# Kernel tuning notes

Measured on AMD Instinct MI355X. Metric: run time of the kernel, lower is better.

The kernel has to match this reference:

```python
import jax, jax.numpy as jnp
import numpy as np

LAYERS = (256, 256, 256)
SPLIT = True


def setup_inputs() -> dict:
    key = jax.random.key(0)
    ks = jax.random.split(key, 4)
    B, F0, D = 512, 40, 32
    # field_num with split=True: [40, 128, 128, 128]
    fnum = [F0]
    for i, s in enumerate(LAYERS):
        fnum.append(s // 2 if (SPLIT and i < len(LAYERS) - 1) else (s // 2 if SPLIT else s))
    # conv input channels per layer: fnum[i] * F0
    c1, c2, c3 = fnum[0] * F0, fnum[1] * F0, fnum[2] * F0  # 1600, 5120, 5120
    inputs = jax.random.normal(ks[0], (B, F0, D), dtype=jnp.float32)
    W1 = jax.random.normal(ks[1], (c1, LAYERS[0]), dtype=jnp.float32) / jnp.sqrt(jnp.float32(c1))
    W2 = jax.random.normal(ks[2], (c2, LAYERS[1]), dtype=jnp.float32) / jnp.sqrt(jnp.float32(c2))
    W3 = jax.random.normal(ks[3], (c3, LAYERS[2]), dtype=jnp.float32) / jnp.sqrt(jnp.float32(c3))
    b1 = jnp.zeros((LAYERS[0],), dtype=jnp.float32)
    b2 = jnp.zeros((LAYERS[1],), dtype=jnp.float32)
    b3 = jnp.zeros((LAYERS[2],), dtype=jnp.float32)
    return {"inputs": inputs, "W1": W1, "b1": b1, "W2": W2, "b2": b2, "W3": W3, "b3": b3}


def _cin_forward(inputs, params):
    # inputs: [B, F0, D]
    B, F0, D = inputs.shape
    x0 = inputs
    h = inputs
    outputs = []
    n = len(params)
    for i, (W, b) in enumerate(params):
        # Per-embedding-dim outer product: [B, D, Fi, F0] -> flatten channels.
        z = jnp.einsum('bfd,bgd->bdfg', h, x0).reshape(B, D, -1)
        # 1x1 Conv1D over length-D axis == dense projection on channel axis.
        y = z @ W + b                     # [B, D, size]
        y = jax.nn.relu(y)
        y = jnp.transpose(y, (0, 2, 1))   # [B, size, D]
        if SPLIT and i < n - 1:
            half = y.shape[1] // 2
            outputs.append(y[:, :half, :])
            h = y[:, half:, :]
        else:
            outputs.append(y)
            h = y
    pooled = jnp.concatenate(outputs, axis=1)  # [B, sum_out_fields, D]
    return jnp.sum(pooled, axis=2)             # [B, sum_out_fields]


def reference(inputs, W1, b1, W2, b2, W3, b3):
    return _cin_forward(inputs, [(W1, b1), (W2, b2), (W3, b3)])
```

## Files before the change

### kernel.cpp

```cpp
#include <hip/hip_runtime.h>
#include <hip/hip_bf16.h>


typedef __attribute__((ext_vector_type(8))) short short8;
typedef __attribute__((ext_vector_type(4))) float f32x4;

#define DEVINL __device__ __forceinline__

DEVINL float bf16f(unsigned short u) {
  return __builtin_bit_cast(float, ((unsigned int)u) << 16);
}
DEVINL unsigned short f2bf(float f) {
  unsigned int u = __builtin_bit_cast(unsigned int, f);
  u = u + 0x7FFFu + ((u >> 16) & 1u);
  return (unsigned short)(u >> 16);
}
DEVINL unsigned int pk2(float lo, float hi) {
  union { __hip_bfloat162 h; unsigned int u; } cv;
  cv.h = __float22bfloat162_rn(make_float2(lo, hi));
  return cv.u;
}
DEVINL void gl_lds16(const unsigned short* g, unsigned short* l) {
  __builtin_amdgcn_global_load_lds(
      (const __attribute__((address_space(1))) unsigned int*)g,
      (__attribute__((address_space(3))) unsigned int*)l, 16, 0, 0);
}

__global__ void prep_x(const float* __restrict__ in, unsigned short* __restrict__ xT) {
  __shared__ float lf[40 * 33];
  const int b = blockIdx.x, t = threadIdx.x;
  for (int i = t; i < 1280; i += 256) {
    int g = i >> 5, d = i & 31;
    lf[g * 33 + d] = in[b * 1280 + i];
  }
  __syncthreads();
  for (int i = t; i < 1280; i += 256) {
    int d = i / 40, g = i % 40;
    xT[b * 1280 + i] = f2bf(lf[g * 33 + d]);
  }
}

__global__ void prep_w(const float* __restrict__ W1, const float* __restrict__ W2,
                       const float* __restrict__ W3, unsigned short* __restrict__ Wf1,
                       unsigned short* __restrict__ Wf2, unsigned short* __restrict__ Wf3) {
  __shared__ float lw[8192];
  const int bid = blockIdx.x, t = threadIdx.x;
  const float* W; unsigned short* dst; int s, SPW;
  if (bid < 50)       { W = W1; dst = Wf1; s = bid;       SPW = 10; }
  else if (bid < 210) { W = W2; dst = Wf2; s = bid - 50;  SPW = 32; }
  else                { W = W3; dst = Wf3; s = bid - 210; SPW = 32; }
  const int smod = s % SPW, w = s / SPW;
  for (int i = t; i < 8192; i += 256) {
    int kl = i >> 8, col = i & 255;
    int f = 4 * smod + (kl >> 3);
    int g = 8 * w + (kl & 7);
    lw[i] = W[(f * 40 + g) * 256 + col];
  }
  __syncthreads();
  for (int c = t; c < 1024; c += 256) {
    int grp = c >> 6, ll = c & 63;
    int qq = ll >> 4, col = grp * 16 + (ll & 15);
    unsigned short u[8];
#pragma unroll
    for (int j = 0; j < 8; ++j) u[j] = f2bf(lw[(qq * 8 + j) * 256 + col]);
    uint4 v;
    v.x = (unsigned)u[0] | ((unsigned)u[1] << 16);
    v.y = (unsigned)u[2] | ((unsigned)u[3] << 16);
    v.z = (unsigned)u[4] | ((unsigned)u[5] << 16);
    v.w = (unsigned)u[6] | ((unsigned)u[7] << 16);
    *(uint4*)&dst[s * 8192 + c * 8] = v;
  }
}

template <int LAYER>
__global__ __launch_bounds__(256, 2) void cin_layer(
    const unsigned short* __restrict__ Wfrag, const unsigned short* __restrict__ xT,
    const unsigned short* __restrict__ hIn, const float* __restrict__ bias,
    unsigned short* __restrict__ hOut, float* __restrict__ out) {
  constexpr int FIN = (LAYER == 1) ? 40 : 128;
  constexpr int NKT = FIN * 40 / 32;
  constexpr int SPW = FIN / 4;
  constexpr int HP = 144;

  constexpr int SM_SHORTS = 16384 + 5120 + ((LAYER > 1) ? 128 * HP : 8);
  __shared__ __align__(16) unsigned short smem[SM_SHORTS];
  unsigned short* Bb = smem;
  unsigned short* xs = smem + 16384;
  unsigned short* hs = smem + 16384 + 5120;

  const int tid = threadIdx.x;
  const int l = tid & 63;
  const int wid = tid >> 6;
  const int q = l >> 4;
  const int bm = blockIdx.x >> 2;
  const int tn = blockIdx.x & 3;
  const int r0 = bm * 128;
  const int b0 = bm * 4;

  const unsigned short* Wbase = Wfrag + tn * 2048 + tid * 8;

#pragma unroll
  for (int s = 0; s < 4; ++s)
    gl_lds16(Wbase + s * 8192, Bb + s * 2048 + tid * 8);
  gl_lds16(xT + r0 * 40 + tid * 8, xs + tid * 8);
  gl_lds16(xT + r0 * 40 + 2048 + tid * 8, xs + 2048 + tid * 8);
  if (tid < 128)
    gl_lds16(xT + r0 * 40 + 4096 + tid * 8, xs + 4096 + tid * 8);
  if constexpr (LAYER > 1) {
    const unsigned short* hsrc = hIn + bm * (128 * HP);
#pragma unroll
    for (int i = 0; i < 9; ++i)
      gl_lds16(hsrc + i * 2048 + tid * 8, hs + i * 2048 + tid * 8);
  }

  f32x4 acc[2][4];
#pragma unroll
  for (int m = 0; m < 2; ++m)
#pragma unroll
    for (int n = 0; n < 4; ++n) acc[m][n] = f32x4{0.f, 0.f, 0.f, 0.f};

  const int rl0 = wid * 32 + (l & 15);

  __syncthreads();

#pragma unroll
  for (int w = 0; w < 5; ++w) {
    float xw[2][8];
#pragma unroll
    for (int mi = 0; mi < 2; ++mi) {
      short8 xv = *(const short8*)&xs[(rl0 + mi * 16) * 40 + w * 8];
#pragma unroll
      for (int d = 0; d < 4; ++d) {
        unsigned int uu = ((const unsigned int*)&xv)[d];
        xw[mi][2 * d]     = __builtin_bit_cast(float, uu << 16);
        xw[mi][2 * d + 1] = __builtin_bit_cast(float, uu & 0xffff0000u);
      }
    }

    for (int sp = 0; sp < SPW / 2; ++sp) {
      const int s0 = w * SPW + 2 * sp;
      __builtin_amdgcn_sched_barrier(0);
      asm volatile("s_waitcnt vmcnt(2)" ::: "memory");
      __builtin_amdgcn_s_barrier();
      __builtin_amdgcn_sched_barrier(0);

      {
        const int sn0 = (s0 + 4 < NKT) ? (s0 + 4) : (NKT - 1);
        const int sn1 = (s0 + 5 < NKT) ? (s0 + 5) : (NKT - 1);
        gl_lds16(Wbase + sn0 * 8192, Bb + ((s0 + 4) & 7) * 2048 + tid * 8);
        gl_lds16(Wbase + sn1 * 8192, Bb + ((s0 + 5) & 7) * 2048 + tid * 8);
      }

#pragma unroll
      for (int half = 0; half < 2; ++half) {
        const int s = s0 + half;
        const int sm = 2 * sp + half;
        const unsigned short* bb = Bb + (s & 7) * 2048 + l * 8;
        short8 bfr[4];
#pragma unroll
        for (int n = 0; n < 4; ++n)
          bfr[n] = *(const short8*)(bb + n * 512);

        const int f = 4 * sm + q;
#pragma unroll
        for (int mi = 0; mi < 2; ++mi) {
          const int rl = rl0 + mi * 16;
          const float hf = (LAYER == 1) ? bf16f(xs[rl * 40 + f])
                                        : bf16f(hs[f * HP + rl]);
          union { unsigned int u[4]; short8 s8; } A;
#pragma unroll
          for (int jj = 0; jj < 4; ++jj)
            A.u[jj] = pk2(hf * xw[mi][2 * jj], hf * xw[mi][2 * jj + 1]);
#pragma unroll
          for (int n = 0; n < 4; ++n)
            acc[mi][n] = __builtin_amdgcn_mfma_f32_16x16x32_bf16(
                A.s8, bfr[n], acc[mi][n], 0, 0, 0);
        }
      }
    }
  }
  asm volatile("s_waitcnt vmcnt(0)" ::: "memory");

  const int colb = tn * 64;
  float bv[4];
#pragma unroll
  for (int n = 0; n < 4; ++n) bv[n] = bias[colb + n * 16 + (l & 15)];

  if (LAYER == 3 || tn < 2) {
    const int jb = (LAYER == 1) ? 0 : (LAYER == 2) ? 128 : 256;
#pragma unroll
    for (int n = 0; n < 4; ++n) {
      const int j = jb + colb + n * 16 + (l & 15);
      float sum = 0.f;
#pragma unroll
      for (int m = 0; m < 2; ++m)
#pragma unroll
        for (int r = 0; r < 4; ++r) sum += fmaxf(acc[m][n][r] + bv[n], 0.f);
      sum += __shfl_xor(sum, 16);
      sum += __shfl_xor(sum, 32);
      if (l < 16) out[(b0 + wid) * 512 + j] = sum;
    }
  } else {
#pragma unroll
    for (int n = 0; n < 4; ++n) {
      const int ff = (tn - 2) * 64 + n * 16 + (l & 15);
#pragma unroll
      for (int m = 0; m < 2; ++m) {
        const int rl = wid * 32 + m * 16 + (l >> 4) * 4;
        float v0 = fmaxf(acc[m][n][0] + bv[n], 0.f);
        float v1 = fmaxf(acc[m][n][1] + bv[n], 0.f);
        float v2 = fmaxf(acc[m][n][2] + bv[n], 0.f);
        float v3 = fmaxf(acc[m][n][3] + bv[n], 0.f);
        uint2 pv;
        pv.x = pk2(v0, v1);
        pv.y = pk2(v2, v3);
        *(uint2*)&hOut[bm * (128 * HP) + ff * HP + rl] = pv;
      }
    }
  }
}

extern "C" void kernel_launch(void* const* d_in, const int* in_sizes, int n_in,
                              void* d_out, int out_size, void* d_ws, size_t ws_size,
                              hipStream_t stream) {
  (void)in_sizes; (void)n_in; (void)out_size; (void)ws_size;
  const float* in = (const float*)d_in[0];
  const float* W1 = (const float*)d_in[1];
  const float* b1 = (const float*)d_in[2];
  const float* W2 = (const float*)d_in[3];
  const float* b2 = (const float*)d_in[4];
  const float* W3 = (const float*)d_in[5];
  const float* b3 = (const float*)d_in[6];
  float* out = (float*)d_out;
  char* ws = (char*)d_ws;

  unsigned short* xT  = (unsigned short*)(ws);
  unsigned short* Wf1 = (unsigned short*)(ws + 1310720);
  unsigned short* Wf2 = (unsigned short*)(ws + 2129920);
  unsigned short* Wf3 = (unsigned short*)(ws + 4751360);
  unsigned short* h1  = (unsigned short*)(ws + 7372800);
  unsigned short* h2  = (unsigned short*)(ws + 12091392);

  prep_x<<<dim3(512), dim3(256), 0, stream>>>(in, xT);
  prep_w<<<dim3(370), dim3(256), 0, stream>>>(W1, W2, W3, Wf1, Wf2, Wf3);
  cin_layer<1><<<dim3(512), dim3(256), 0, stream>>>(Wf1, xT, (const unsigned short*)nullptr, b1, h1, out);
  cin_layer<2><<<dim3(512), dim3(256), 0, stream>>>(Wf2, xT, h1, b2, h2, out);
  cin_layer<3><<<dim3(512), dim3(256), 0, stream>>>(Wf3, xT, h2, b3, (unsigned short*)nullptr, out);
}
```

Before: 200.6 us.

## Double waves per block so each wave computes one 16-row M tile

Each CIN layer block now runs 512 threads (8 waves) instead of 256 (4 waves). Each wave owns 16 rows instead of 32, which halves its accumulators and its A-fragment construction per step. Global-to-LDS loads for the weight pipeline are split across the two halves of the block, so each thread issues one prefetch per step and the wait count drops to 1. Pairs of waves combine their row-sum partials through LDS before writing the pooled output. A manual round-to-nearest-even bf16 pack replaces the intrinsic pack for the A operand. The change aims for more latency hiding and less per-wave VALU work, at the cost of an extra block-wide barrier and more waves sharing the same B fragments loaded from LDS.

Measured after the change: 225.6 us. 1.12x slower.

```diff
diff --git a/kernel.cpp b/kernel.cpp
--- a/kernel.cpp
+++ b/kernel.cpp
@@ -19,6 +19,13 @@
   union { __hip_bfloat162 h; unsigned int u; } cv;
   cv.h = __float22bfloat162_rn(make_float2(lo, hi));
   return cv.u;
+}
+DEVINL unsigned int pkrne(float a, float b) {
+  unsigned int ua = __builtin_bit_cast(unsigned int, a);
+  unsigned int ub = __builtin_bit_cast(unsigned int, b);
+  ua = ua + 0x7FFFu + ((ua >> 16) & 1u);
+  ub = ub + 0x7FFFu + ((ub >> 16) & 1u);
+  return (ua >> 16) | (ub & 0xFFFF0000u);
 }
 DEVINL void gl_lds16(const unsigned short* g, unsigned short* l) {
   __builtin_amdgcn_global_load_lds(
@@ -73,7 +80,7 @@
 }
 
 template <int LAYER>
-__global__ __launch_bounds__(256, 2) void cin_layer(
+__global__ __launch_bounds__(512, 4) void cin_layer(
     const unsigned short* __restrict__ Wfrag, const unsigned short* __restrict__ xT,
     const unsigned short* __restrict__ hIn, const float* __restrict__ bias,
     unsigned short* __restrict__ hOut, float* __restrict__ out) {
@@ -90,65 +97,67 @@
 
   const int tid = threadIdx.x;
   const int l = tid & 63;
-  const int wid = tid >> 6;
+  const int wv = tid >> 6;
   const int q = l >> 4;
   const int bm = blockIdx.x >> 2;
   const int tn = blockIdx.x & 3;
   const int r0 = bm * 128;
   const int b0 = bm * 4;
 
-  const unsigned short* Wbase = Wfrag + tn * 2048 + tid * 8;
-
-#pragma unroll
-  for (int s = 0; s < 4; ++s)
-    gl_lds16(Wbase + s * 8192, Bb + s * 2048 + tid * 8);
+  const int sel = tid >> 8;
+  const int idx = tid & 255;
+
+#pragma unroll
+  for (int r = 0; r < 2; ++r) {
+    const int i2 = r * 512 + tid;
+    const int sl = i2 >> 8;
+    gl_lds16(Wfrag + sl * 8192 + tn * 2048 + (i2 & 255) * 8, Bb + i2 * 8);
+  }
   gl_lds16(xT + r0 * 40 + tid * 8, xs + tid * 8);
-  gl_lds16(xT + r0 * 40 + 2048 + tid * 8, xs + 2048 + tid * 8);
   if (tid < 128)
     gl_lds16(xT + r0 * 40 + 4096 + tid * 8, xs + 4096 + tid * 8);
   if constexpr (LAYER > 1) {
     const unsigned short* hsrc = hIn + bm * (128 * HP);
 #pragma unroll
-    for (int i = 0; i < 9; ++i)
-      gl_lds16(hsrc + i * 2048 + tid * 8, hs + i * 2048 + tid * 8);
-  }
-
-  f32x4 acc[2][4];
-#pragma unroll
-  for (int m = 0; m < 2; ++m)
-#pragma unroll
-    for (int n = 0; n < 4; ++n) acc[m][n] = f32x4{0.f, 0.f, 0.f, 0.f};
-
-  const int rl0 = wid * 32 + (l & 15);
+    for (int i = 0; i < 4; ++i)
+      gl_lds16(hsrc + i * 4096 + tid * 8, hs + i * 4096 + tid * 8);
+    if (tid < 256)
+      gl_lds16(hsrc + 16384 + tid * 8, hs + 16384 + tid * 8);
+  }
+
+  f32x4 acc[4];
+#pragma unroll
+  for (int n = 0; n < 4; ++n) acc[n] = f32x4{0.f, 0.f, 0.f, 0.f};
+
+  const int rl0 = wv * 16 + (l & 15);
 
   __syncthreads();
 
 #pragma unroll
   for (int w = 0; w < 5; ++w) {
-    float xw[2][8];
-#pragma unroll
-    for (int mi = 0; mi < 2; ++mi) {
-      short8 xv = *(const short8*)&xs[(rl0 + mi * 16) * 40 + w * 8];
+    float xw[8];
+    {
+      short8 xv = *(const short8*)&xs[rl0 * 40 + w * 8];
 #pragma unroll
       for (int d = 0; d < 4; ++d) {
         unsigned int uu = ((const unsigned int*)&xv)[d];
-        xw[mi][2 * d]     = __builtin_bit_cast(float, uu << 16);
-        xw[mi][2 * d + 1] = __builtin_bit_cast(float, uu & 0xffff0000u);
+        xw[2 * d]     = __builtin_bit_cast(float, uu << 16);
+        xw[2 * d + 1] = __builtin_bit_cast(float, uu & 0xffff0000u);
       }
     }
 
     for (int sp = 0; sp < SPW / 2; ++sp) {
       const int s0 = w * SPW + 2 * sp;
       __builtin_amdgcn_sched_barrier(0);
-      asm volatile("s_waitcnt vmcnt(2)" ::: "memory");
+      asm volatile("s_waitcnt vmcnt(1)" ::: "memory");
       __builtin_amdgcn_s_barrier();
       __builtin_amdgcn_sched_barrier(0);
 
       {
-        const int sn0 = (s0 + 4 < NKT) ? (s0 + 4) : (NKT - 1);
-        const int sn1 = (s0 + 5 < NKT) ? (s0 + 5) : (NKT - 1);
-        gl_lds16(Wbase + sn0 * 8192, Bb + ((s0 + 4) & 7) * 2048 + tid * 8);
-        gl_lds16(Wbase + sn1 * 8192, Bb + ((s0 + 5) & 7) * 2048 + tid * 8);
+        const int stp = s0 + 4 + sel;
+        const int stc = (stp < NKT) ? stp : (NKT - 1);
+        gl_lds16(Wfrag + stc * 8192 + tn * 2048 + idx * 8,
+                 Bb + (stp & 7) * 2048 + idx * 8);
       }
 
 #pragma unroll
@@ -162,20 +171,16 @@
           bfr[n] = *(const short8*)(bb + n * 512);
 
         const int f = 4 * sm + q;
-#pragma unroll
-        for (int mi = 0; mi < 2; ++mi) {
-          const int rl = rl0 + mi * 16;
-          const float hf = (LAYER == 1) ? bf16f(xs[rl * 40 + f])
-                                        : bf16f(hs[f * HP + rl]);
-          union { unsigned int u[4]; short8 s8; } A;
-#pragma unroll
-          for (int jj = 0; jj < 4; ++jj)
-            A.u[jj] = pk2(hf * xw[mi][2 * jj], hf * xw[mi][2 * jj + 1]);
-#pragma unroll
-          for (int n = 0; n < 4; ++n)
-            acc[mi][n] = __builtin_amdgcn_mfma_f32_16x16x32_bf16(
-                A.s8, bfr[n], acc[mi][n], 0, 0, 0);
-        }
+        const float hf = (LAYER == 1) ? bf16f(xs[rl0 * 40 + f])
+                                      : bf16f(hs[f * HP + rl0]);
+        union { unsigned int u[4]; short8 s8; } A;
+#pragma unroll
+        for (int jj = 0; jj < 4; ++jj)
+          A.u[jj] = pkrne(hf * xw[2 * jj], hf * xw[2 * jj + 1]);
+#pragma unroll
+        for (int n = 0; n < 4; ++n)
+          acc[n] = __builtin_amdgcn_mfma_f32_16x16x32_bf16(
+              A.s8, bfr[n], acc[n], 0, 0, 0);
       }
     }
   }
@@ -188,34 +193,45 @@
 
   if (LAYER == 3 || tn < 2) {
     const int jb = (LAYER == 1) ? 0 : (LAYER == 2) ? 128 : 256;
+    float psum[4];
 #pragma unroll
     for (int n = 0; n < 4; ++n) {
-      const int j = jb + colb + n * 16 + (l & 15);
-      float sum = 0.f;
-#pragma unroll
-      for (int m = 0; m < 2; ++m)
-#pragma unroll
-        for (int r = 0; r < 4; ++r) sum += fmaxf(acc[m][n][r] + bv[n], 0.f);
-      sum += __shfl_xor(sum, 16);
-      sum += __shfl_xor(sum, 32);
-      if (l < 16) out[(b0 + wid) * 512 + j] = sum;
+      float s = 0.f;
+#pragma unroll
+      for (int r = 0; r < 4; ++r) s += fmaxf(acc[n][r] + bv[n], 0.f);
+      s += __shfl_xor(s, 16);
+      s += __shfl_xor(s, 32);
+      psum[n] = s;
+    }
+    __syncthreads();
+    float* sred = (float*)xs;
+    if (wv & 1) {
+      if (l < 16)
+#pragma unroll
+        for (int n = 0; n < 4; ++n)
+          sred[((wv >> 1) * 4 + n) * 16 + l] = psum[n];
+    }
+    __syncthreads();
+    if (!(wv & 1) && l < 16) {
+#pragma unroll
+      for (int n = 0; n < 4; ++n) {
+        float tot = psum[n] + sred[((wv >> 1) * 4 + n) * 16 + l];
+        out[(b0 + (wv >> 1)) * 512 + jb + colb + n * 16 + l] = tot;
+      }
     }
   } else {
 #pragma unroll
     for (int n = 0; n < 4; ++n) {
       const int ff = (tn - 2) * 64 + n * 16 + (l & 15);
-#pragma unroll
-      for (int m = 0; m < 2; ++m) {
-        const int rl = wid * 32 + m * 16 + (l >> 4) * 4;
-        float v0 = fmaxf(acc[m][n][0] + bv[n], 0.f);
-        float v1 = fmaxf(acc[m][n][1] + bv[n], 0.f);
-        float v2 = fmaxf(acc[m][n][2] + bv[n], 0.f);
-        float v3 = fmaxf(acc[m][n][3] + bv[n], 0.f);
-        uint2 pv;
-        pv.x = pk2(v0, v1);
-        pv.y = pk2(v2, v3);
-        *(uint2*)&hOut[bm * (128 * HP) + ff * HP + rl] = pv;
-      }
+      const int rl = wv * 16 + (l >> 4) * 4;
+      float v0 = fmaxf(acc[n][0] + bv[n], 0.f);
+      float v1 = fmaxf(acc[n][1] + bv[n], 0.f);
+      float v2 = fmaxf(acc[n][2] + bv[n], 0.f);
+      float v3 = fmaxf(acc[n][3] + bv[n], 0.f);
+      uint2 pv;
+      pv.x = pk2(v0, v1);
+      pv.y = pk2(v2, v3);
+      *(uint2*)&hOut[bm * (128 * HP) + ff * HP + rl] = pv;
     }
   }
 }
@@ -243,7 +259,7 @@
 
   prep_x<<<dim3(512), dim3(256), 0, stream>>>(in, xT);
   prep_w<<<dim3(370), dim3(256), 0, stream>>>(W1, W2, W3, Wf1, Wf2, Wf3);
-  cin_layer<1><<<dim3(512), dim3(256), 0, stream>>>(Wf1, xT, (const unsigned short*)nullptr, b1, h1, out);
-  cin_layer<2><<<dim3(512), dim3(256), 0, stream>>>(Wf2, xT, h1, b2, h2, out);
-  cin_layer<3><<<dim3(512), dim3(256), 0, stream>>>(Wf3, xT, h2, b3, (unsigned short*)nullptr, out);
-}
+  cin_layer<1><<<dim3(512), dim3(512), 0, stream>>>(Wf1, xT, (const unsigned short*)nullptr, b1, h1, out);
+  cin_layer<2><<<dim3(512), dim3(512), 0, stream>>>(Wf2, xT, h1, b2, h2, out);
+  cin_layer<3><<<dim3(512), dim3(512), 0, stream>>>(Wf3, xT, h2, b3, (unsigned short*)nullptr, out);
+}
```
